# Optimization experiments

Measured on AMD Instinct MI355X. Metric: run time of the kernel, lower is better.

The kernel has to match this reference:

```python
import jax, jax.numpy as jnp
import numpy as np

NODE_DIM = 64
DEPTH = 2
N = 50000          # node_size
DEG = 24           # average degree
E = N * DEG        # triple_size = 1.2M edges
R = 500            # rel_size
FEAT = NODE_DIM * (DEPTH + 1)  # 192


def _l2norm(x, eps=1e-12):
    # torch F.normalize(p=2): x / max(||x||, eps)
    n = jnp.sqrt(jnp.sum(x * x, axis=-1, keepdims=True))
    return x / jnp.maximum(n, eps)


def setup_inputs() -> dict:
    key = jax.random.key(0)
    ks = jax.random.split(key, 8)
    features = jax.random.normal(ks[0], (N, NODE_DIM), jnp.float32)
    rel_emb = jax.random.normal(ks[1], (R, NODE_DIM), jnp.float32)
    # duplicate-free edge list, rows sorted (matches a coalesced sparse adj)
    rows = jnp.repeat(jnp.arange(N, dtype=jnp.int32), DEG)
    offs = jnp.tile(1 + jnp.arange(DEG, dtype=jnp.int32) * 7, N)
    cols = (rows + offs) % N
    adj = jnp.stack([rows, cols])  # [2, E]
    # sparse [E, R] triple->relation matrix: one relation per triple
    r_index = jnp.stack([jnp.arange(E, dtype=jnp.int32),
                         jax.random.randint(ks[2], (E,), 0, R, jnp.int32)])
    r_val = jax.random.uniform(ks[3], (E,), jnp.float32, 0.5, 1.5)
    # params (xavier-ish scales)
    proxy = jax.random.normal(ks[4], (64, FEAT), jnp.float32) * (1.0 / np.sqrt(FEAT))
    gate_w = jax.random.normal(ks[5], (FEAT, FEAT), jnp.float32) * (1.0 / np.sqrt(FEAT))
    gate_b = jnp.zeros((FEAT,), jnp.float32)
    attn_kernels = jax.random.normal(ks[6], (DEPTH, NODE_DIM), jnp.float32) * 0.1
    return {"features": features, "rel_emb": rel_emb, "proxy": proxy,
            "gate_w": gate_w, "gate_b": gate_b, "attn_kernels": attn_kernels,
            "adj": adj, "r_index": r_index, "r_val": r_val,
            "triple_size": E, "rel_size": R, "node_size": N}


def reference(features, rel_emb, proxy, gate_w, gate_b, attn_kernels,
              adj, r_index, r_val, triple_size, rel_size, node_size):
    feats = jnp.tanh(features)
    outs = [feats]
    dst = adj[0]  # rows: softmax / scatter-sum segment ids
    src = adj[1]  # cols: neighbor gather ids
    for l in range(attn_kernels.shape[0]):
        neighs = feats[src]                                  # [E, d] gather
        # sparse.mm(tri_rel, rel_emb): sum_k r_val * rel_emb[rel_id] per triple
        tri_rel = jax.ops.segment_sum(r_val[:, None] * rel_emb[r_index[1]],
                                      r_index[0], num_segments=triple_size)
        tri_rel = _l2norm(tri_rel)                           # [E, d]
        # relational reflection: h - 2 <h, r> r
        neighs = neighs - 2.0 * jnp.sum(neighs * tri_rel, axis=1, keepdims=True) * tri_rel
        att = jnp.einsum('ed,d->e', tri_rel, attn_kernels[l])  # [E]
        # sparse softmax over rows of adjacency (segment softmax over dst)
        m = jax.ops.segment_max(att, dst, num_segments=node_size)
        ex = jnp.exp(att - m[dst])
        denom = jax.ops.segment_sum(ex, dst, num_segments=node_size)
        w = ex / denom[dst]
        new_f = jax.ops.segment_sum(neighs * w[:, None], dst, num_segments=node_size)
        feats = jnp.tanh(new_f)
        outs.append(feats)
    outputs = jnp.concatenate(outs, axis=-1)                 # [N, feat]
    proxy_att = jax.nn.softmax(_l2norm(outputs) @ _l2norm(proxy).T, axis=-1)
    proxy_feature = outputs - proxy_att @ proxy
    gate = jax.nn.sigmoid(proxy_feature @ gate_w.T + gate_b)
    return gate * outputs + (1.0 - gate) * proxy_feature
```

## Files before the change

### kernel.cpp

```cpp
#include <hip/hip_runtime.h>
#include <hip/hip_bf16.h>
#include <cstdint>
#include <cstddef>

#define N_NODES 50000
#define DEG     24
#define NEDGE   (N_NODES*DEG)
#define RSZ     500
#define NDIM    64
#define FEATD   192

#define PASTR   72

#define LGRID   1568
#define LCHUNK  196

typedef short bf16x8 __attribute__((ext_vector_type(8)));
typedef float f32x4  __attribute__((ext_vector_type(4)));

__device__ __forceinline__ unsigned short f2bf(float f) {
    unsigned u = __builtin_bit_cast(unsigned, f);
    unsigned r = (u + 0x7fffu + ((u >> 16) & 1u)) >> 16;
    return (unsigned short)r;
}
__device__ __forceinline__ float bf2f(unsigned short s) {
    unsigned u = ((unsigned)s) << 16;
    return __builtin_bit_cast(float, u);
}
__device__ __forceinline__ float lo16(unsigned u) {
    return __builtin_bit_cast(float, u << 16);
}
__device__ __forceinline__ float hi16(unsigned u) {
    return __builtin_bit_cast(float, u & 0xFFFF0000u);
}
__device__ __forceinline__ float fast_tanh(float x) {
    float e = __expf(2.f * x);
    return 1.f - 2.f / (e + 1.f);
}

__global__ __launch_bounds__(256) void k_prep(const float* __restrict__ features,
                                              const float* __restrict__ rel_emb,
                                              const float* __restrict__ attn_k,
                                              const float* __restrict__ proxy,
                                              const float* __restrict__ gate_w,
                                              const int* __restrict__ src,
                                              const int* __restrict__ rel,
                                              unsigned short* __restrict__ fin0,
                                              float* __restrict__ reln,
                                              float* __restrict__ expdot,
                                              float* __restrict__ pninv,
                                              unsigned short* __restrict__ B1,
                                              unsigned short* __restrict__ B2,
                                              unsigned short* __restrict__ B3,
                                              unsigned short* __restrict__ B4,
                                              unsigned int* __restrict__ pedge) {
    int b = blockIdx.x;
    if (b < 3125) {
        int t = b * 256 + threadIdx.x;
        int idx4 = t * 4;
        float4 f = *reinterpret_cast<const float4*>(features + idx4);
        uint2 w;
        w.x = (unsigned)f2bf(fast_tanh(f.x)) | ((unsigned)f2bf(fast_tanh(f.y)) << 16);
        w.y = (unsigned)f2bf(fast_tanh(f.z)) | ((unsigned)f2bf(fast_tanh(f.w)) << 16);
        *reinterpret_cast<uint2*>(fin0 + idx4) = w;
    } else if (b < 3250) {
        int lane = threadIdx.x & 63;
        int row = (b - 3125) * 4 + (threadIdx.x >> 6);
        float v = rel_emb[row * 64 + lane];
        float ss = v * v;
        for (int m = 1; m < 64; m <<= 1) ss += __shfl_xor(ss, m);
        float inv = 1.f / fmaxf(sqrtf(ss), 1e-12f);
        float rn = v * inv;
        reln[row * 64 + lane] = rn;
        float d0 = rn * attn_k[lane];
        float d1 = rn * attn_k[64 + lane];
        for (int m = 1; m < 64; m <<= 1) { d0 += __shfl_xor(d0, m); d1 += __shfl_xor(d1, m); }
        if (lane == 0) { expdot[row] = __expf(d0); expdot[RSZ + row] = __expf(d1); }
    } else if (b < 3266) {
        int lane = threadIdx.x & 63;
        int row = (b - 3250) * 4 + (threadIdx.x >> 6);
        const float* p = proxy + (size_t)row * FEATD;
        float a = p[lane], bb = p[64 + lane], c = p[128 + lane];
        float ss = a * a + bb * bb + c * c;
        for (int m = 1; m < 64; m <<= 1) ss += __shfl_xor(ss, m);
        if (lane == 0) pninv[row] = 1.f / fmaxf(sqrtf(ss), 1e-12f);
    } else if (b < 3506) {
        int idx = (b - 3266) * 256 + threadIdx.x;
        int j = idx & 7, lane = (idx >> 3) & 63;
        int t = idx >> 9;
        int lane16 = lane & 15, quad = lane >> 4;
        if (t < 24) {
            int kt = t >> 2, nt = t & 3;
            int k = kt * 32 + quad * 8 + j, n = nt * 16 + lane16;
            B1[idx] = f2bf(proxy[(size_t)n * FEATD + k]);
        } else if (t < 48) {
            int tt = t - 24, kt = tt / 12, nt = tt % 12;
            int k = kt * 32 + quad * 8 + j, n = nt * 16 + lane16;
            B2[idx - 12288] = f2bf(proxy[(size_t)k * FEATD + n]);
        } else {
            int tt = t - 48, kt = tt / 12, nt = tt % 12;
            int k = kt * 32 + quad * 8 + j, n = nt * 16 + lane16;
            B3[idx - 24576] = f2bf(gate_w[(size_t)n * FEATD + k]);
        }
    } else if (b < 4678) {
        int t = (b - 3506) * 256 + threadIdx.x;
        if (t < NEDGE / 4) {
            int4 s4 = *reinterpret_cast<const int4*>(src + t * 4);
            int4 r4 = *reinterpret_cast<const int4*>(rel + t * 4);
            uint4 o;
            o.x = (unsigned)s4.x | ((unsigned)r4.x << 16);
            o.y = (unsigned)s4.y | ((unsigned)r4.y << 16);
            o.z = (unsigned)s4.z | ((unsigned)r4.z << 16);
            o.w = (unsigned)s4.w | ((unsigned)r4.w << 16);
            *reinterpret_cast<uint4*>(pedge + t * 4) = o;
        }
    } else {
        int t = (b - 4678) * 256 + threadIdx.x;
        int j = t & 7, lane = (t >> 3) & 63, tl = t >> 9;
        int lane16 = lane & 15, quad = lane >> 4;
        int kt = tl / 12, nt = tl % 12;
        int k = kt * 32 + quad * 8 + j, n = nt * 16 + lane16;
        const float4* pr = reinterpret_cast<const float4*>(proxy + (size_t)k * FEATD);
        const float4* gr = reinterpret_cast<const float4*>(gate_w + (size_t)n * FEATD);
        float acc = 0.f;
#pragma unroll 8
        for (int q = 0; q < 48; q++) {
            float4 a = pr[q], g4 = gr[q];
            acc += a.x * g4.x + a.y * g4.y + a.z * g4.z + a.w * g4.w;
        }
        B4[t] = f2bf(acc);
    }
}

__global__ __launch_bounds__(256) void k_layer(const unsigned int* __restrict__ pedge,
                                               const float* __restrict__ reln,
                                               const float* __restrict__ expdot_l,
                                               const unsigned short* __restrict__ fin,
                                               unsigned short* __restrict__ fout) {
    int b = blockIdx.x;
    int lb = (b & 7) * LCHUNK + (b >> 3);
    int lane8 = threadIdx.x & 7;
    int node = lb * 32 + (threadIdx.x >> 3);
    if (node >= N_NODES) return;
    int ebase = node * DEG;
    unsigned pk[DEG];
#pragma unroll
    for (int k = 0; k < DEG; k++) pk[k] = pedge[ebase + k];
    float a0 = 0.f, a1 = 0.f, a2 = 0.f, a3 = 0.f;
    float a4 = 0.f, a5 = 0.f, a6 = 0.f, a7 = 0.f, den = 0.f;
#pragma unroll 4
    for (int k = 0; k < DEG; k++) {
        unsigned p = pk[k];
        int s = p & 0xFFFF;
        int r = p >> 16;
        float ex = expdot_l[r];
        const float* tp = reln + (size_t)r * 64 + lane8 * 8;
        float4 t0 = *reinterpret_cast<const float4*>(tp);
        float4 t1v = *reinterpret_cast<const float4*>(tp + 4);
        uint4 u = *reinterpret_cast<const uint4*>(fin + (size_t)s * 64 + lane8 * 8);
        float n0 = lo16(u.x), n1 = hi16(u.x), n2 = lo16(u.y), n3 = hi16(u.y);
        float n4 = lo16(u.z), n5 = hi16(u.z), n6 = lo16(u.w), n7 = hi16(u.w);
        float pd = t0.x * n0 + t0.y * n1 + t0.z * n2 + t0.w * n3
                 + t1v.x * n4 + t1v.y * n5 + t1v.z * n6 + t1v.w * n7;
        pd += __shfl_xor(pd, 1); pd += __shfl_xor(pd, 2); pd += __shfl_xor(pd, 4);
        float t1 = -2.f * pd * ex;
        a0 = fmaf(ex, n0, fmaf(t1, t0.x, a0));
        a1 = fmaf(ex, n1, fmaf(t1, t0.y, a1));
        a2 = fmaf(ex, n2, fmaf(t1, t0.z, a2));
        a3 = fmaf(ex, n3, fmaf(t1, t0.w, a3));
        a4 = fmaf(ex, n4, fmaf(t1, t1v.x, a4));
        a5 = fmaf(ex, n5, fmaf(t1, t1v.y, a5));
        a6 = fmaf(ex, n6, fmaf(t1, t1v.z, a6));
        a7 = fmaf(ex, n7, fmaf(t1, t1v.w, a7));
        den += ex;
    }
    float id = 1.f / den;
    uint4 w;
    w.x = (unsigned)f2bf(fast_tanh(a0 * id)) | ((unsigned)f2bf(fast_tanh(a1 * id)) << 16);
    w.y = (unsigned)f2bf(fast_tanh(a2 * id)) | ((unsigned)f2bf(fast_tanh(a3 * id)) << 16);
    w.z = (unsigned)f2bf(fast_tanh(a4 * id)) | ((unsigned)f2bf(fast_tanh(a5 * id)) << 16);
    w.w = (unsigned)f2bf(fast_tanh(a6 * id)) | ((unsigned)f2bf(fast_tanh(a7 * id)) << 16);
    *reinterpret_cast<uint4*>(fout + (size_t)node * 64 + lane8 * 8) = w;
}

__global__ __launch_bounds__(256) void k_gate(const unsigned short* __restrict__ fin0,
                                              const unsigned short* __restrict__ fin1,
                                              const unsigned short* __restrict__ fin2,
                                              const unsigned short* __restrict__ B1,
                                              const unsigned short* __restrict__ B2,
                                              const unsigned short* __restrict__ B3,
                                              const unsigned short* __restrict__ B4,
                                              const float* __restrict__ pninv,
                                              const float* __restrict__ gate_b,
                                              float* __restrict__ dout) {
    __shared__ unsigned short lds[4][16 * PASTR];
    int wv = threadIdx.x >> 6, lane = threadIdx.x & 63;
    int tile = blockIdx.x * 4 + wv;
    if (tile > N_NODES / 16 - 1) tile = N_NODES / 16 - 1;
    int row0 = tile * 16, lane16 = lane & 15, quad = lane >> 4;
    unsigned short* L = lds[wv];
    const unsigned short* fsel[3] = {fin0, fin1, fin2};

    bf16x8 af[6];
    float ss = 0.f;
#pragma unroll
    for (int kt = 0; kt < 6; kt++) {
        const unsigned short* f = fsel[kt >> 1];
        bf16x8 a = *reinterpret_cast<const bf16x8*>(f + (size_t)(row0 + lane16) * 64 + (kt & 1) * 32 + quad * 8);
        af[kt] = a;
#pragma unroll
        for (int i = 0; i < 8; i++) {
            float v = bf2f((unsigned short)a[i]);
            ss = fmaf(v, v, ss);
        }
    }
    ss += __shfl_xor(ss, 16); ss += __shfl_xor(ss, 32);
    float inv = 1.f / fmaxf(sqrtf(ss), 1e-12f);
    float pni[4];
#pragma unroll
    for (int nt = 0; nt < 4; nt++) pni[nt] = pninv[nt * 16 + lane16];
    f32x4 acc4[4];
#pragma unroll
    for (int nt = 0; nt < 4; nt++) acc4[nt] = (f32x4){0.f, 0.f, 0.f, 0.f};
#pragma unroll
    for (int kt = 0; kt < 6; kt++) {
#pragma unroll
        for (int nt = 0; nt < 4; nt++) {
            bf16x8 bfr = *reinterpret_cast<const bf16x8*>(B1 + ((size_t)(kt * 4 + nt) * 64 + lane) * 8);
            acc4[nt] = __builtin_amdgcn_mfma_f32_16x16x32_bf16(af[kt], bfr, acc4[nt], 0, 0, 0);
        }
    }
#pragma unroll
    for (int r = 0; r < 4; r++) {
        int rowloc = quad * 4 + r;
        float invr = __shfl(inv, rowloc);
        float e0 = __expf(acc4[0][r] * invr * pni[0]);
        float e1 = __expf(acc4[1][r] * invr * pni[1]);
        float e2 = __expf(acc4[2][r] * invr * pni[2]);
        float e3 = __expf(acc4[3][r] * invr * pni[3]);
        float s = e0 + e1 + e2 + e3;
        s += __shfl_xor(s, 1); s += __shfl_xor(s, 2);
        s += __shfl_xor(s, 4); s += __shfl_xor(s, 8);
        float rs = 1.f / s;
        L[rowloc * PASTR + lane16]      = f2bf(e0 * rs);
        L[rowloc * PASTR + 16 + lane16] = f2bf(e1 * rs);
        L[rowloc * PASTR + 32 + lane16] = f2bf(e2 * rs);
        L[rowloc * PASTR + 48 + lane16] = f2bf(e3 * rs);
    }
    __threadfence_block();

    bf16x8 paf0 = *reinterpret_cast<const bf16x8*>(L + lane16 * PASTR + quad * 8);
    bf16x8 paf1 = *reinterpret_cast<const bf16x8*>(L + lane16 * PASTR + 32 + quad * 8);

#pragma unroll
    for (int c = 0; c < 4; c++) {
        int nt0 = c * 3;
        f32x4 s3[3], s4[3], s2[3];
#pragma unroll
        for (int n = 0; n < 3; n++) {
            s3[n] = (f32x4){0.f, 0.f, 0.f, 0.f};
            s4[n] = (f32x4){0.f, 0.f, 0.f, 0.f};
            s2[n] = (f32x4){0.f, 0.f, 0.f, 0.f};
        }
        float och[3][4];
#pragma unroll
        for (int n = 0; n < 3; n++) {
            const unsigned short* f = fsel[(nt0 + n) >> 2];
#pragma unroll
            for (int r = 0; r < 4; r++)
                och[n][r] = bf2f(f[(size_t)(row0 + quad * 4 + r) * 64 + ((nt0 + n) & 3) * 16 + lane16]);
        }
#pragma unroll
        for (int kt = 0; kt < 6; kt++) {
#pragma unroll
            for (int n = 0; n < 3; n++) {
                bf16x8 bfr = *reinterpret_cast<const bf16x8*>(B3 + ((size_t)(kt * 12 + nt0 + n) * 64 + lane) * 8);
                s3[n] = __builtin_amdgcn_mfma_f32_16x16x32_bf16(af[kt], bfr, s3[n], 0, 0, 0);
            }
        }
#pragma unroll
        for (int n = 0; n < 3; n++) {
            bf16x8 b40 = *reinterpret_cast<const bf16x8*>(B4 + ((size_t)(nt0 + n) * 64 + lane) * 8);
            bf16x8 b41 = *reinterpret_cast<const bf16x8*>(B4 + ((size_t)(12 + nt0 + n) * 64 + lane) * 8);
            s4[n] = __builtin_amdgcn_mfma_f32_16x16x32_bf16(paf0, b40, s4[n], 0, 0, 0);
            s4[n] = __builtin_amdgcn_mfma_f32_16x16x32_bf16(paf1, b41, s4[n], 0, 0, 0);
            bf16x8 b20 = *reinterpret_cast<const bf16x8*>(B2 + ((size_t)(nt0 + n) * 64 + lane) * 8);
            bf16x8 b21 = *reinterpret_cast<const bf16x8*>(B2 + ((size_t)(12 + nt0 + n) * 64 + lane) * 8);
            s2[n] = __builtin_amdgcn_mfma_f32_16x16x32_bf16(paf0, b20, s2[n], 0, 0, 0);
            s2[n] = __builtin_amdgcn_mfma_f32_16x16x32_bf16(paf1, b21, s2[n], 0, 0, 0);
        }
#pragma unroll
        for (int n = 0; n < 3; n++) {
            int nt = nt0 + n;
            float bias = gate_b[nt * 16 + lane16];
#pragma unroll
            for (int r = 0; r < 4; r++) {
                int rowloc = quad * 4 + r;
                float z = s3[n][r] - s4[n][r] + bias;
                float g = 1.f / (1.f + __expf(-z));
                dout[(size_t)(row0 + rowloc) * FEATD + nt * 16 + lane16] =
                    och[n][r] - (1.f - g) * s2[n][r];
            }
        }
    }
}

extern "C" void kernel_launch(void* const* d_in, const int* in_sizes, int n_in,
                              void* d_out, int out_size, void* d_ws, size_t ws_size,
                              hipStream_t stream) {
    (void)in_sizes; (void)n_in; (void)out_size; (void)ws_size;
    const float* features = (const float*)d_in[0];
    const float* rel_emb  = (const float*)d_in[1];
    const float* proxy    = (const float*)d_in[2];
    const float* gate_w   = (const float*)d_in[3];
    const float* gate_b   = (const float*)d_in[4];
    const float* attn_k   = (const float*)d_in[5];
    const int*   adj      = (const int*)d_in[6];
    const int*   r_index  = (const int*)d_in[7];

    unsigned short* fin0 = (unsigned short*)d_ws;
    unsigned short* fin1 = fin0 + (size_t)N_NODES * 64;
    unsigned short* fin2 = fin1 + (size_t)N_NODES * 64;
    float* reln    = (float*)(fin2 + (size_t)N_NODES * 64);
    float* expdot  = reln + RSZ * 64;
    float* pninv   = expdot + 2 * RSZ;
    unsigned short* B1 = (unsigned short*)(pninv + 64);
    unsigned short* B2 = B1 + 12288;
    unsigned short* B3 = B2 + 12288;
    unsigned short* B4 = B3 + 36864;
    unsigned int* pedge = (unsigned int*)(B4 + 12288);

    const int* src = adj + NEDGE;
    const int* rel = r_index + NEDGE;

    k_prep  <<<dim3(4726), dim3(256), 0, stream>>>(features, rel_emb, attn_k, proxy, gate_w,
                                                   src, rel, fin0, reln, expdot,
                                                   pninv, B1, B2, B3, B4, pedge);
    k_layer <<<dim3(LGRID), dim3(256), 0, stream>>>(pedge, reln, expdot,       fin0, fin1);
    k_layer <<<dim3(LGRID), dim3(256), 0, stream>>>(pedge, reln, expdot + RSZ, fin1, fin2);
    k_gate  <<<dim3(782),  dim3(256), 0, stream>>>(fin0, fin1, fin2, B1, B2, B3, B4, pninv,
                                                   gate_b, (float*)d_out);
}
```

Baseline: 191.7 us.

## Split gate output columns across two waves per tile and extract outputs via identity MFMA

Each 16-row tile in the gate kernel is now handled by two waves, each producing half of the 192 output columns, which doubles the grid and shortens per-wave serial work. The per-column reload of the layer outputs from global memory is replaced by an MFMA against an identity matrix, which pulls the already-loaded A fragments into accumulator layout. The cost is that both waves redo the A loads, the norm and the proxy softmax, and the extra MFMA must reproduce the values exactly.

```diff
diff --git a/kernel.cpp b/kernel.cpp
--- a/kernel.cpp
+++ b/kernel.cpp
@@ -9,6 +9,7 @@
 #define RSZ     500
 #define NDIM    64
 #define FEATD   192
+#define NTILES  (N_NODES/16)
 
 #define PASTR   72
 
@@ -195,8 +196,10 @@
                                               float* __restrict__ dout) {
     __shared__ unsigned short lds[4][16 * PASTR];
     int wv = threadIdx.x >> 6, lane = threadIdx.x & 63;
-    int tile = blockIdx.x * 4 + wv;
-    if (tile > N_NODES / 16 - 1) tile = N_NODES / 16 - 1;
+    int g = blockIdx.x * 4 + wv;
+    int tile = g >> 1;
+    if (tile > NTILES - 1) tile = NTILES - 1;
+    int half = g & 1;
     int row0 = tile * 16, lane16 = lane & 15, quad = lane >> 4;
     unsigned short* L = lds[wv];
     const unsigned short* fsel[3] = {fin0, fin1, fin2};
@@ -252,23 +255,24 @@
     bf16x8 paf0 = *reinterpret_cast<const bf16x8*>(L + lane16 * PASTR + quad * 8);
     bf16x8 paf1 = *reinterpret_cast<const bf16x8*>(L + lane16 * PASTR + 32 + quad * 8);
 
-#pragma unroll
-    for (int c = 0; c < 4; c++) {
-        int nt0 = c * 3;
-        f32x4 s3[3], s4[3], s2[3];
+    bf16x8 i0, i1;
+#pragma unroll
+    for (int j = 0; j < 8; j++) {
+        int k = quad * 8 + j;
+        i0[j] = (short)((k == lane16)      ? 0x3F80 : 0);
+        i1[j] = (short)((k == lane16 + 16) ? 0x3F80 : 0);
+    }
+
+#pragma unroll
+    for (int c = 0; c < 2; c++) {
+        int nt0 = half * 6 + c * 3;
+        f32x4 s3[3], s4[3], s2[3], oc[3];
 #pragma unroll
         for (int n = 0; n < 3; n++) {
             s3[n] = (f32x4){0.f, 0.f, 0.f, 0.f};
             s4[n] = (f32x4){0.f, 0.f, 0.f, 0.f};
             s2[n] = (f32x4){0.f, 0.f, 0.f, 0.f};
-        }
-        float och[3][4];
-#pragma unroll
-        for (int n = 0; n < 3; n++) {
-            const unsigned short* f = fsel[(nt0 + n) >> 2];
-#pragma unroll
-            for (int r = 0; r < 4; r++)
-                och[n][r] = bf2f(f[(size_t)(row0 + quad * 4 + r) * 64 + ((nt0 + n) & 3) * 16 + lane16]);
+            oc[n] = (f32x4){0.f, 0.f, 0.f, 0.f};
         }
 #pragma unroll
         for (int kt = 0; kt < 6; kt++) {
@@ -280,14 +284,16 @@
         }
 #pragma unroll
         for (int n = 0; n < 3; n++) {
-            bf16x8 b40 = *reinterpret_cast<const bf16x8*>(B4 + ((size_t)(nt0 + n) * 64 + lane) * 8);
-            bf16x8 b41 = *reinterpret_cast<const bf16x8*>(B4 + ((size_t)(12 + nt0 + n) * 64 + lane) * 8);
+            int nt = nt0 + n;
+            bf16x8 b40 = *reinterpret_cast<const bf16x8*>(B4 + ((size_t)nt * 64 + lane) * 8);
+            bf16x8 b41 = *reinterpret_cast<const bf16x8*>(B4 + ((size_t)(12 + nt) * 64 + lane) * 8);
             s4[n] = __builtin_amdgcn_mfma_f32_16x16x32_bf16(paf0, b40, s4[n], 0, 0, 0);
             s4[n] = __builtin_amdgcn_mfma_f32_16x16x32_bf16(paf1, b41, s4[n], 0, 0, 0);
-            bf16x8 b20 = *reinterpret_cast<const bf16x8*>(B2 + ((size_t)(nt0 + n) * 64 + lane) * 8);
-            bf16x8 b21 = *reinterpret_cast<const bf16x8*>(B2 + ((size_t)(12 + nt0 + n) * 64 + lane) * 8);
+            bf16x8 b20 = *reinterpret_cast<const bf16x8*>(B2 + ((size_t)nt * 64 + lane) * 8);
+            bf16x8 b21 = *reinterpret_cast<const bf16x8*>(B2 + ((size_t)(12 + nt) * 64 + lane) * 8);
             s2[n] = __builtin_amdgcn_mfma_f32_16x16x32_bf16(paf0, b20, s2[n], 0, 0, 0);
             s2[n] = __builtin_amdgcn_mfma_f32_16x16x32_bf16(paf1, b21, s2[n], 0, 0, 0);
+            oc[n] = __builtin_amdgcn_mfma_f32_16x16x32_bf16(af[nt >> 1], (nt & 1) ? i1 : i0, oc[n], 0, 0, 0);
         }
 #pragma unroll
         for (int n = 0; n < 3; n++) {
@@ -297,9 +303,9 @@
             for (int r = 0; r < 4; r++) {
                 int rowloc = quad * 4 + r;
                 float z = s3[n][r] - s4[n][r] + bias;
-                float g = 1.f / (1.f + __expf(-z));
+                float gg = 1.f / (1.f + __expf(-z));
                 dout[(size_t)(row0 + rowloc) * FEATD + nt * 16 + lane16] =
-                    och[n][r] - (1.f - g) * s2[n][r];
+                    oc[n][r] - (1.f - gg) * s2[n][r];
             }
         }
     }
@@ -338,6 +344,6 @@
                                                    pninv, B1, B2, B3, B4, pedge);
     k_layer <<<dim3(LGRID), dim3(256), 0, stream>>>(pedge, reln, expdot,       fin0, fin1);
     k_layer <<<dim3(LGRID), dim3(256), 0, stream>>>(pedge, reln, expdot + RSZ, fin1, fin2);
-    k_gate  <<<dim3(782),  dim3(256), 0, stream>>>(fin0, fin1, fin2, B1, B2, B3, B4, pninv,
+    k_gate  <<<dim3(1563), dim3(256), 0, stream>>>(fin0, fin1, fin2, B1, B2, B3, B4, pninv,
                                                    gate_b, (float*)d_out);
 }
```

After: 234.8 us. +22.5%, slower.
